# Performance work log

Hardware: AMD Instinct MI355X
Metric: run time of the kernel (lower is better)

Reference implementation:

```python
import jax, jax.numpy as jnp
import numpy as np

L = 2          # num_layers
B = 32         # batch
T = 64         # max_sequence_length (= source len here)
H = 1024       # hidden_size
E = 1024       # embedding_size (== H so layer weights stack uniformly)
V = 16000      # vocab (in == out)


def _cell(x, h, c, Wih, Whh, bih, bhh):
    # PyTorch LSTM gate order: i, f, g, o
    g = x @ Wih.T + h @ Whh.T + (bih + bhh)
    i, f, gg, o = jnp.split(g, 4, axis=-1)
    c_new = jax.nn.sigmoid(f) * c + jax.nn.sigmoid(i) * jnp.tanh(gg)
    h_new = jax.nn.sigmoid(o) * jnp.tanh(c_new)
    return h_new, c_new


def _stack_step(h, c, x, Wih, Whh, bih, bhh):
    # h, c: (L, B, H); x: (B, E). Fixed small loop over layers.
    hs, cs, inp = [], [], x
    for l in range(L):
        nh, nc = _cell(inp, h[l], c[l], Wih[l], Whh[l], bih[l], bhh[l])
        hs.append(nh); cs.append(nc); inp = nh
    return jnp.stack(hs), jnp.stack(cs), inp


def setup_inputs() -> dict:
    key = jax.random.key(0)
    ks = jax.random.split(key, 16)
    s = 1.0 / np.sqrt(H)
    U = lambda k, shp: jax.random.uniform(k, shp, jnp.float32, -s, s)
    inp = {
        "input_ids": jax.random.randint(ks[0], (B, T), 0, V),
        "output_ids": jax.random.randint(ks[1], (B, T), 0, V),
        "enc_emb": jax.random.normal(ks[2], (V, E), jnp.float32),
        "enc_Wih": U(ks[3], (L, 4 * H, H)),
        "enc_Whh": U(ks[4], (L, 4 * H, H)),
        "enc_bih": U(ks[5], (L, 4 * H)),
        "enc_bhh": U(ks[6], (L, 4 * H)),
        "dec_emb": jax.random.normal(ks[7], (V, E), jnp.float32),
        "dec_Wih": U(ks[8], (L, 4 * H, H)),
        "dec_Whh": U(ks[9], (L, 4 * H, H)),
        "dec_bih": U(ks[10], (L, 4 * H)),
        "dec_bhh": U(ks[11], (L, 4 * H)),
        "Wout": U(ks[12], (V, H)),
        "bout": U(ks[13], (V,)),
    }
    return inp


def reference(input_ids, output_ids, enc_emb, enc_Wih, enc_Whh, enc_bih, enc_bhh,
              dec_emb, dec_Wih, dec_Whh, dec_bih, dec_bhh, Wout, bout):
    dtype = enc_emb.dtype
    # ---- Encoder: run LSTM over source, keep final (h, c) ----
    enc_x = enc_emb[input_ids]                      # (B, T, E); dropout is identity (eval)
    h0 = jnp.zeros((L, B, H), dtype)
    c0 = jnp.zeros((L, B, H), dtype)

    def enc_step(carry, xt):
        h, c = carry
        h, c, _ = _stack_step(h, c, xt, enc_Wih, enc_Whh, enc_bih, enc_bhh)
        return (h, c), None

    (h, c), _ = jax.lax.scan(enc_step, (h0, c0), jnp.swapaxes(enc_x, 0, 1))

    # ---- Decoder: teacher-forced; step i consumes output_ids[:, i-1] ----
    dec_x = dec_emb[output_ids[:, : T - 1]]         # (B, T-1, E)

    def dec_step(carry, xt):
        h, c = carry
        h, c, top = _stack_step(h, c, xt, dec_Wih, dec_Whh, dec_bih, dec_bhh)
        logit = top @ Wout.T + bout                  # (B, V)
        return (h, c), logit

    (_, _), logits_seq = jax.lax.scan(dec_step, (h, c), jnp.swapaxes(dec_x, 0, 1))

    # ---- Assemble logits like the torch code ----
    logits = jnp.zeros((B, T, V), dtype)
    # torch: logits[:, 0, output_ids[:, 0]] = 1  (broadcasts over both batch dims)
    logits = logits.at[:, 0, output_ids[:, 0]].set(1.0)
    logits = logits.at[:, 1:, :].set(jnp.swapaxes(logits_seq, 0, 1))
    return logits
```

## Files before the change

kernel.cpp:

```cpp
#include <hip/hip_runtime.h>

namespace {

constexpr int kB = 32;
constexpr int kT = 64;
constexpr int kH = 1024;
constexpr int kE = 1024;
constexpr int kV = 16000;
constexpr int kG = 4096;

typedef __attribute__((ext_vector_type(8))) short short8v;
typedef __attribute__((ext_vector_type(4))) float f32x4;

__device__ __forceinline__ float sigmoid_f(float x) {
  return 1.0f / (1.0f + __expf(-x));
}
__device__ __forceinline__ unsigned short f2bf(float x) {
  unsigned int u = __builtin_bit_cast(unsigned int, x);
  u = (u + 0x7FFFu + ((u >> 16) & 1u)) >> 16;
  return (unsigned short)u;
}
__device__ __forceinline__ float bf2f(unsigned short h) {
  return __builtin_bit_cast(float, (unsigned int)h << 16);
}

__global__ void zero_t0_kernel(float* __restrict__ out) {
  int idx = blockIdx.x * blockDim.x + threadIdx.x;
  if (idx >= kB * kV) return;
  int b = idx / kV, v = idx % kV;
  __builtin_nontemporal_store(0.0f, &out[(size_t)b * kT * kV + v]);
}

__global__ void ones_t0_kernel(const int* __restrict__ output_ids,
                               float* __restrict__ out) {
  int b = threadIdx.x >> 5;
  int j = threadIdx.x & 31;
  int id = output_ids[j * kT];
  out[(size_t)b * kT * kV + id] = 1.0f;
}

struct ConvJobs {
  const float* src[8];
  unsigned short* dst[8];
  int mode[8];
};
__global__ __launch_bounds__(256)
void conv8(ConvJobs C) {
  const int mat = blockIdx.x >> 11;
  const int idx = (blockIdx.x & 2047) * 256 + threadIdx.x;
  const float* __restrict__ src = C.src[mat];
  unsigned short* __restrict__ dst = C.dst[mat];
  const int l = idx & 63;
  int row, k;
  if (C.mode[mat] == 0) {
    const int kstep = (idx >> 6) & 31;
    const int uq = (idx >> 11) & 1;
    const int ub = idx >> 12;
    const int n = l & 15;
    row = (n >> 2) * kH + ub * 8 + uq * 4 + (n & 3);
    k = kstep * 32 + ((l >> 4) << 3);
  } else {
    const int s = (idx >> 6) & 31;
    const int rg = idx >> 11;
    row = rg * 16 + (l & 15);
    k = s * 32 + ((l >> 4) << 3);
  }
  const float4* p = reinterpret_cast<const float4*>(src + (size_t)row * kH + k);
  float4 v0 = p[0], v1 = p[1];
  short8v o;
  o[0] = (short)f2bf(v0.x); o[1] = (short)f2bf(v0.y);
  o[2] = (short)f2bf(v0.z); o[3] = (short)f2bf(v0.w);
  o[4] = (short)f2bf(v1.x); o[5] = (short)f2bf(v1.y);
  o[6] = (short)f2bf(v1.z); o[7] = (short)f2bf(v1.w);
  *reinterpret_cast<short8v*>(dst + (size_t)idx * 8) = o;
}

__global__ __launch_bounds__(256)
void convert_frag(const float* __restrict__ src, unsigned short* __restrict__ dst,
                  int nchunks) {
  const int idx = blockIdx.x * 256 + threadIdx.x;
  if (idx >= nchunks) return;
  const int lane = idx & 63;
  const int s = (idx >> 6) & 31;
  const int rg = idx >> 11;
  const int row = rg * 16 + (lane & 15);
  const int k = s * 32 + ((lane >> 4) << 3);
  const float4* p = reinterpret_cast<const float4*>(src + (size_t)row * kH + k);
  float4 v0 = p[0], v1 = p[1];
  short8v o;
  o[0] = (short)f2bf(v0.x); o[1] = (short)f2bf(v0.y);
  o[2] = (short)f2bf(v0.z); o[3] = (short)f2bf(v0.w);
  o[4] = (short)f2bf(v1.x); o[5] = (short)f2bf(v1.y);
  o[6] = (short)f2bf(v1.z); o[7] = (short)f2bf(v1.w);
  *reinterpret_cast<short8v*>(dst + (size_t)idx * 8) = o;
}

__global__ void bias_cell(const float* __restrict__ bih,
                          const float* __restrict__ bhh, float* __restrict__ dst) {
  const int i = blockIdx.x * 256 + threadIdx.x;
  if (i >= kG) return;
  const int g = i >> 10, u = i & 1023;
  dst[(u >> 2) * 16 + g * 4 + (u & 3)] = bih[i] + bhh[i];
}

__global__ __launch_bounds__(256)
void gather_frag(const float* __restrict__ emb, const int* __restrict__ ids,
                 unsigned short* __restrict__ dst, int ntiles) {
  const int idx = blockIdx.x * 256 + threadIdx.x;
  const int lane = idx & 63;
  const int s = (idx >> 6) & 31;
  const int tile = idx >> 11;
  if (tile >= ntiles) return;
  const int m = tile * 16 + (lane & 15);
  const int t = m >> 5, b = m & 31;
  const int id = ids[b * kT + t];
  const int k = s * 32 + ((lane >> 4) << 3);
  const float4* p = reinterpret_cast<const float4*>(emb + (size_t)id * kE + k);
  float4 v0 = p[0], v1 = p[1];
  short8v o;
  o[0] = (short)f2bf(v0.x); o[1] = (short)f2bf(v0.y);
  o[2] = (short)f2bf(v0.z); o[3] = (short)f2bf(v0.w);
  o[4] = (short)f2bf(v1.x); o[5] = (short)f2bf(v1.y);
  o[6] = (short)f2bf(v1.z); o[7] = (short)f2bf(v1.w);
  *reinterpret_cast<short8v*>(dst + (size_t)idx * 8) = o;
}

__global__ __launch_bounds__(256)
void proj_mfma(const unsigned short* __restrict__ Af,
               const unsigned short* __restrict__ Bf,
               const float* __restrict__ b0, const float* __restrict__ b1,
               unsigned short* __restrict__ dst, int nmt) {
  const int w = threadIdx.x >> 6, lane = threadIdx.x & 63;
  const int mg = blockIdx.x, ng = blockIdx.y;
  f32x4 acc[4][2] = {};
  const unsigned short* Ab[4];
  const unsigned short* Bb[2];
#pragma unroll
  for (int i = 0; i < 4; ++i) {
    int tile = mg * 4 + i;
    if (tile > nmt - 1) tile = nmt - 1;
    Ab[i] = Af + (size_t)tile * 16384 + lane * 8;
  }
#pragma unroll
  for (int j = 0; j < 2; ++j) {
    const int nt = ng * 8 + w * 2 + j;
    Bb[j] = Bf + (size_t)nt * 16384 + lane * 8;
  }
#pragma unroll 2
  for (int s = 0; s < 32; ++s) {
    short8v a[4], b[2];
#pragma unroll
    for (int i = 0; i < 4; ++i) a[i] = *reinterpret_cast<const short8v*>(Ab[i] + s * 512);
#pragma unroll
    for (int j = 0; j < 2; ++j) b[j] = *reinterpret_cast<const short8v*>(Bb[j] + s * 512);
#pragma unroll
    for (int i = 0; i < 4; ++i)
#pragma unroll
      for (int j = 0; j < 2; ++j)
        acc[i][j] = __builtin_amdgcn_mfma_f32_16x16x32_bf16(a[i], b[j], acc[i][j], 0, 0, 0);
  }
#pragma unroll
  for (int i = 0; i < 4; ++i) {
    const int tile = mg * 4 + i;
    if (tile >= nmt) continue;
    const int mbase = tile * 16 + ((lane >> 4) << 2);
#pragma unroll
    for (int j = 0; j < 2; ++j) {
      const int n = (ng * 8 + w * 2 + j) * 16 + (lane & 15);
      const float bj = b0[n] + b1[n];
      const int g = n >> 10;
      const int u = n & 1023;
      const int q = u >> 2;
      const int uu = u & 3;
#pragma unroll
      for (int r = 0; r < 4; ++r) {
        const int m2 = mbase + r;
        const int t = m2 >> 5, mb = m2 & 31;
        dst[(size_t)t * kB * kG + (size_t)(q * 32 + mb) * 16 + g * 4 + uu] =
            f2bf(acc[i][j][r] + bj);
      }
    }
  }
}

__global__ __launch_bounds__(256)
void out_gemm_mfma(const unsigned short* __restrict__ Af,
                   const unsigned short* __restrict__ Bf,
                   const float* __restrict__ bias, float* __restrict__ out) {
  const int w = threadIdx.x >> 6, lane = threadIdx.x & 63;
  const int bid = blockIdx.x;
  const int swz = (bid & 7) * 252 + (bid >> 3);
  const int mg = swz & 31, ng = swz >> 5;
  __shared__ float LsF[32 * 260];
  f32x4 acc[4][4] = {};
  const unsigned short* Ab[4];
  const unsigned short* Bb[4];
#pragma unroll
  for (int i = 0; i < 4; ++i) {
    int tile = mg * 4 + i;
    if (tile > 125) tile = 125;
    Ab[i] = Af + (size_t)tile * 16384 + lane * 8;
  }
#pragma unroll
  for (int j = 0; j < 4; ++j) {
    int nt = ng * 16 + w * 4 + j;
    if (nt > 999) nt = 999;
    Bb[j] = Bf + (size_t)nt * 16384 + lane * 8;
  }
#pragma unroll 2
  for (int s = 0; s < 32; ++s) {
    short8v a[4], b[4];
#pragma unroll
    for (int i = 0; i < 4; ++i) a[i] = *reinterpret_cast<const short8v*>(Ab[i] + s * 512);
#pragma unroll
    for (int j = 0; j < 4; ++j) b[j] = *reinterpret_cast<const short8v*>(Bb[j] + s * 512);
#pragma unroll
    for (int i = 0; i < 4; ++i)
#pragma unroll
      for (int j = 0; j < 4; ++j)
        acc[i][j] = __builtin_amdgcn_mfma_f32_16x16x32_bf16(a[i], b[j], acc[i][j], 0, 0, 0);
  }
  const int nglob = ng * 256 + lane * 4;
  f32x4 b4 = {0.f, 0.f, 0.f, 0.f};
  if (nglob < kV) b4 = *reinterpret_cast<const f32x4*>(&bias[nglob]);
#pragma unroll
  for (int ph = 0; ph < 2; ++ph) {
    if (ph) __syncthreads();
#pragma unroll
    for (int i2 = 0; i2 < 2; ++i2) {
      const int i = ph * 2 + i2;
      const int r2b = i2 * 16 + ((lane >> 4) << 2);
#pragma unroll
      for (int j = 0; j < 4; ++j) {
        const int nloc = (w * 4 + j) * 16 + (lane & 15);
#pragma unroll
        for (int r = 0; r < 4; ++r) LsF[(r2b + r) * 260 + nloc] = acc[i][j][r];
      }
    }
    __syncthreads();
    if (nglob < kV) {
#pragma unroll
      for (int it = 0; it < 8; ++it) {
        const int r2l = w * 8 + it;
        const int m = mg * 64 + ph * 32 + r2l;
        if (m >= 2016) break;
        f32x4 v = *reinterpret_cast<const f32x4*>(&LsF[r2l * 260 + lane * 4]);
        v += b4;
        const int sd = m >> 5, bb = m & 31;
        f32x4* dst = reinterpret_cast<f32x4*>(
            &out[(size_t)bb * kT * kV + (size_t)(sd + 1) * kV + nglob]);
        __builtin_nontemporal_store(v, dst);
      }
    }
  }
}

struct RecurArgs {
  const unsigned short* wih1[2];
  const unsigned short* whh1[2];
  const unsigned short* whh0[2];
  const unsigned short* xproj[2];
  const float* bsum1[2];
  unsigned short* h0seq;
  unsigned short* h1seq;
  int* flags;
};

#define LOADW(dst, src)                                                      \
  {                                                                          \
    _Pragma("unroll") for (int s_ = 0; s_ < 4; ++s_) dst[s_] =               \
        *reinterpret_cast<const short8v*>((src) + wbase + (size_t)s_ * 512); \
  }

__global__ __launch_bounds__(512, 1)
void lstm_persist(RecurArgs A) {
  const int q = blockIdx.x;
  const int tid = threadIdx.x;
  const int wave = tid >> 6, lane = tid & 63;
  const int ksb = wave * 4;
  __shared__ alignas(16) float Ls[3][8][2][64][4];

  const size_t wbase = ((size_t)(q * 32 + ksb) * 64 + lane) * 8;
  short8v wI[4], wJ[4], wH[4];
  LOADW(wI, A.wih1[0]);
  LOADW(wJ, A.whh1[0]);
  LOADW(wH, A.whh0[0]);

  const int m = (tid < 128) ? (tid >> 2) : 0;
  const int ul = tid & 3;
  const int u = q * 4 + ul;
  float cold0 = 0.f, cold1 = 0.f;
  float bs[4];
  if (tid < 128) {
#pragma unroll
    for (int g = 0; g < 4; ++g) bs[g] = A.bsum1[0][q * 16 + g * 4 + ul];
  }
  const int mt = m >> 4, r = m & 3;
  const int lm = (m & 12) << 2;
  const int ksu = u >> 5;
  const int lane3 = (m & 15) | (((u >> 3) & 3) << 4);
  const int e = u & 7;
  const size_t fidx = (size_t)((mt * 32 + ksu) * 64 + lane3) * 8 + e;

  for (int p = 0; p < 128; ++p) {
    if (p == 64) LOADW(wH, A.whh0[1]);
    if (p == 65) {
      LOADW(wI, A.wih1[1]);
      LOADW(wJ, A.whh1[1]);
      if (tid < 128) {
#pragma unroll
        for (int g = 0; g < 4; ++g) bs[g] = A.bsum1[1][q * 16 + g * 4 + ul];
      }
    }
    float xp[4] = {};
    if (tid < 128 && p <= 126) {
      const int e0 = (p < kT) ? 0 : 1;
      const unsigned short* xprojc =
          A.xproj[e0] + (size_t)(e0 ? (p - kT) : p) * kB * kG;
#pragma unroll
      for (int g = 0; g < 4; ++g)
        xp[g] = bf2f(xprojc[(q * 32 + m) * 16 + g * 4 + ul]);
    }

    const unsigned short* A0 = A.h0seq + (size_t)p * 32768;
    const unsigned short* A1 = A.h1seq + (size_t)(p > 0 ? p - 1 : 0) * 32768;

    f32x4 aI0 = {0.f, 0.f, 0.f, 0.f}, aI1 = {0.f, 0.f, 0.f, 0.f};
    f32x4 aJ0 = {0.f, 0.f, 0.f, 0.f}, aJ1 = {0.f, 0.f, 0.f, 0.f};
    f32x4 aH0 = {0.f, 0.f, 0.f, 0.f}, aH1 = {0.f, 0.f, 0.f, 0.f};
#pragma unroll
    for (int s = 0; s < 4; ++s) {
      const int ks = ksb + s;
      const short8v a00 =
          *reinterpret_cast<const short8v*>(A0 + (size_t)(ks * 64 + lane) * 8);
      const short8v a01 =
          *reinterpret_cast<const short8v*>(A0 + (size_t)((32 + ks) * 64 + lane) * 8);
      const short8v a10 =
          *reinterpret_cast<const short8v*>(A1 + (size_t)(ks * 64 + lane) * 8);
      const short8v a11 =
          *reinterpret_cast<const short8v*>(A1 + (size_t)((32 + ks) * 64 + lane) * 8);
      aI0 = __builtin_amdgcn_mfma_f32_16x16x32_bf16(a00, wI[s], aI0, 0, 0, 0);
      aI1 = __builtin_amdgcn_mfma_f32_16x16x32_bf16(a01, wI[s], aI1, 0, 0, 0);
      aJ0 = __builtin_amdgcn_mfma_f32_16x16x32_bf16(a10, wJ[s], aJ0, 0, 0, 0);
      aJ1 = __builtin_amdgcn_mfma_f32_16x16x32_bf16(a11, wJ[s], aJ1, 0, 0, 0);
      aH0 = __builtin_amdgcn_mfma_f32_16x16x32_bf16(a00, wH[s], aH0, 0, 0, 0);
      aH1 = __builtin_amdgcn_mfma_f32_16x16x32_bf16(a01, wH[s], aH1, 0, 0, 0);
    }
    *reinterpret_cast<f32x4*>(&Ls[0][wave][0][lane][0]) = aI0;
    *reinterpret_cast<f32x4*>(&Ls[0][wave][1][lane][0]) = aI1;
    *reinterpret_cast<f32x4*>(&Ls[1][wave][0][lane][0]) = aJ0;
    *reinterpret_cast<f32x4*>(&Ls[1][wave][1][lane][0]) = aJ1;
    *reinterpret_cast<f32x4*>(&Ls[2][wave][0][lane][0]) = aH0;
    *reinterpret_cast<f32x4*>(&Ls[2][wave][1][lane][0]) = aH1;
    __syncthreads();

    if (tid < 128) {
      if (p <= 126) {
        float g0[4];
#pragma unroll
        for (int g = 0; g < 4; ++g) {
          const int ln = (g * 4 + ul) | lm;
          float v = 0.f;
#pragma unroll
          for (int ww = 0; ww < 8; ++ww) v += Ls[2][ww][mt][ln][r];
          g0[g] = v + xp[g];
        }
        const float cnew = sigmoid_f(g0[1]) * cold0 + sigmoid_f(g0[0]) * tanhf(g0[2]);
        const float hnew = sigmoid_f(g0[3]) * tanhf(cnew);
        cold0 = cnew;
        const unsigned int hb = f2bf(hnew);
        const unsigned int other = __shfl_xor((int)hb, 1);
        if ((ul & 1) == 0) {
          unsigned int word = (hb & 0xffffu) | (other << 16);
          unsigned int* dst = reinterpret_cast<unsigned int*>(
              A.h0seq + (size_t)(p + 1) * 32768 + fidx);
          __hip_atomic_store(dst, word, __ATOMIC_RELAXED,
                             __HIP_MEMORY_SCOPE_AGENT);
        }
      }
      if (p >= 1) {
        float g1[4];
#pragma unroll
        for (int g = 0; g < 4; ++g) {
          const int ln = (g * 4 + ul) | lm;
          float v = 0.f;
#pragma unroll
          for (int ww = 0; ww < 8; ++ww)
            v += Ls[0][ww][mt][ln][r] + Ls[1][ww][mt][ln][r];
          g1[g] = v + bs[g];
        }
        const float cnew = sigmoid_f(g1[1]) * cold1 + sigmoid_f(g1[0]) * tanhf(g1[2]);
        const float hnew = sigmoid_f(g1[3]) * tanhf(cnew);
        cold1 = cnew;
        const unsigned int hb = f2bf(hnew);
        const unsigned int other = __shfl_xor((int)hb, 1);
        if ((ul & 1) == 0) {
          unsigned int word = (hb & 0xffffu) | (other << 16);
          unsigned int* dst = reinterpret_cast<unsigned int*>(
              A.h1seq + (size_t)p * 32768 + fidx);
          __hip_atomic_store(dst, word, __ATOMIC_RELAXED,
                             __HIP_MEMORY_SCOPE_AGENT);
        }
      }
    }

    asm volatile("s_waitcnt vmcnt(0)" ::: "memory");
    __syncthreads();
    if (tid == 0)
      __hip_atomic_store(&A.flags[q], p + 1, __ATOMIC_RELAXED,
                         __HIP_MEMORY_SCOPE_AGENT);
    if (wave == 0) {
      const int fb = lane * 4;
      for (int guard = 0; guard < (1 << 17); ++guard) {
        int f0 = __hip_atomic_load(&A.flags[fb + 0], __ATOMIC_RELAXED,
                                   __HIP_MEMORY_SCOPE_AGENT);
        int f1 = __hip_atomic_load(&A.flags[fb + 1], __ATOMIC_RELAXED,
                                   __HIP_MEMORY_SCOPE_AGENT);
        int f2 = __hip_atomic_load(&A.flags[fb + 2], __ATOMIC_RELAXED,
                                   __HIP_MEMORY_SCOPE_AGENT);
        int f3 = __hip_atomic_load(&A.flags[fb + 3], __ATOMIC_RELAXED,
                                   __HIP_MEMORY_SCOPE_AGENT);
        const int mn = min(min(f0, f1), min(f2, f3));
        if (__all(mn > p)) break;
        __builtin_amdgcn_s_sleep(2);
      }
    }
    __syncthreads();
  }
}

}

extern "C" void kernel_launch(void* const* d_in, const int* in_sizes, int n_in,
                              void* d_out, int out_size, void* d_ws, size_t ws_size,
                              hipStream_t stream) {
  const int* input_ids = (const int*)d_in[0];
  const int* output_ids = (const int*)d_in[1];
  const float* enc_emb = (const float*)d_in[2];
  const float* enc_Wih = (const float*)d_in[3];
  const float* enc_Whh = (const float*)d_in[4];
  const float* enc_bih = (const float*)d_in[5];
  const float* enc_bhh = (const float*)d_in[6];
  const float* dec_emb = (const float*)d_in[7];
  const float* dec_Wih = (const float*)d_in[8];
  const float* dec_Whh = (const float*)d_in[9];
  const float* dec_bih = (const float*)d_in[10];
  const float* dec_bhh = (const float*)d_in[11];
  const float* Wout = (const float*)d_in[12];
  const float* bout = (const float*)d_in[13];
  float* out = (float*)d_out;
  char* ws = (char*)d_ws;

  const size_t WL = (size_t)kG * kH;

  size_t off = 0;
  unsigned short* wout_frag = (unsigned short*)(ws + 0);
  unsigned short* xproj_enc = (unsigned short*)(ws + off); off += (size_t)kT * kB * kG * 2;
  unsigned short* xin_enc = (unsigned short*)(ws + off);
  unsigned short* h0seq = xin_enc;
  off += (size_t)kT * kB * kH * 2;
  unsigned short* wih0_enc = (unsigned short*)(ws + off); off += WL * 2;
  unsigned short* wih0_dec = (unsigned short*)(ws + off); off += WL * 2;
  unsigned short* xproj_dec = (unsigned short*)(ws + off); off += (size_t)(kT - 1) * kB * kG * 2;
  unsigned short* xin_dec = (unsigned short*)(ws + off); off += (size_t)(kT - 1) * kB * kH * 2;
  unsigned short* h1seq = (unsigned short*)(ws + off); off += (size_t)128 * kB * kH * 2;
  unsigned short* wswz[6];
  for (int i = 0; i < 6; ++i) { wswz[i] = (unsigned short*)(ws + off); off += WL * 2; }
  float* bsum_enc = (float*)(ws + off); off += kG * 4;
  float* bsum_dec = (float*)(ws + off); off += kG * 4;
  int* flags = (int*)(ws + off); off += 1024;

  ConvJobs C;
  C.src[0] = enc_Whh;       C.dst[0] = wswz[0];    C.mode[0] = 0;
  C.src[1] = enc_Wih + WL;  C.dst[1] = wswz[1];    C.mode[1] = 0;
  C.src[2] = enc_Whh + WL;  C.dst[2] = wswz[2];    C.mode[2] = 0;
  C.src[3] = dec_Whh;       C.dst[3] = wswz[3];    C.mode[3] = 0;
  C.src[4] = dec_Wih + WL;  C.dst[4] = wswz[4];    C.mode[4] = 0;
  C.src[5] = dec_Whh + WL;  C.dst[5] = wswz[5];    C.mode[5] = 0;
  C.src[6] = enc_Wih;       C.dst[6] = wih0_enc;   C.mode[6] = 1;
  C.src[7] = dec_Wih;       C.dst[7] = wih0_dec;   C.mode[7] = 1;
  conv8<<<8 * 2048, 256, 0, stream>>>(C);
  bias_cell<<<16, 256, 0, stream>>>(enc_bih + kG, enc_bhh + kG, bsum_enc);
  bias_cell<<<16, 256, 0, stream>>>(dec_bih + kG, dec_bhh + kG, bsum_dec);

  gather_frag<<<128 * 8, 256, 0, stream>>>(enc_emb, input_ids, xin_enc, 128);
  gather_frag<<<126 * 8, 256, 0, stream>>>(dec_emb, output_ids, xin_dec, 126);

  proj_mfma<<<dim3(32, 32), 256, 0, stream>>>(xin_enc, wih0_enc, enc_bih, enc_bhh,
                                              xproj_enc, 128);
  proj_mfma<<<dim3(32, 32), 256, 0, stream>>>(xin_dec, wih0_dec, dec_bih, dec_bhh,
                                              xproj_dec, 126);

  (void)hipMemsetAsync(h0seq, 0, (size_t)kB * kH * 2, stream);
  (void)hipMemsetAsync(h1seq, 0, (size_t)kB * kH * 2, stream);
  (void)hipMemsetAsync(flags, 0, 1024, stream);

  RecurArgs RA;
  RA.wih1[0] = wswz[1]; RA.wih1[1] = wswz[4];
  RA.whh1[0] = wswz[2]; RA.whh1[1] = wswz[5];
  RA.whh0[0] = wswz[0]; RA.whh0[1] = wswz[3];
  RA.xproj[0] = xproj_enc; RA.xproj[1] = xproj_dec;
  RA.bsum1[0] = bsum_enc; RA.bsum1[1] = bsum_dec;
  RA.h0seq = h0seq;
  RA.h1seq = h1seq;
  RA.flags = flags;
  lstm_persist<<<256, 512, 0, stream>>>(RA);

  convert_frag<<<8000, 256, 0, stream>>>(Wout, wout_frag, kV * (kH / 8));

  zero_t0_kernel<<<(kB * kV + 255) / 256, 256, 0, stream>>>(out);
  ones_t0_kernel<<<1, kB * kB, 0, stream>>>(output_ids, out);

  out_gemm_mfma<<<2016, 256, 0, stream>>>(h1seq + (size_t)65 * kB * kH,
                                          wout_frag, bout, out);
}
```

Measured before the change: 1.178 ms.

## Use per-step atomic counter barrier and shrink output GEMM shared staging

```diff
diff --git a/kernel.cpp b/kernel.cpp
--- a/kernel.cpp
+++ b/kernel.cpp
@@ -183,7 +183,7 @@
   }
 }
 
-__global__ __launch_bounds__(256)
+__global__ __launch_bounds__(256, 5)
 void out_gemm_mfma(const unsigned short* __restrict__ Af,
                    const unsigned short* __restrict__ Bf,
                    const float* __restrict__ bias, float* __restrict__ out) {
@@ -191,7 +191,7 @@
   const int bid = blockIdx.x;
   const int swz = (bid & 7) * 252 + (bid >> 3);
   const int mg = swz & 31, ng = swz >> 5;
-  __shared__ float LsF[32 * 260];
+  __shared__ float LsF[16 * 260];
   f32x4 acc[4][4] = {};
   const unsigned short* Ab[4];
   const unsigned short* Bb[4];
@@ -224,32 +224,29 @@
   f32x4 b4 = {0.f, 0.f, 0.f, 0.f};
   if (nglob < kV) b4 = *reinterpret_cast<const f32x4*>(&bias[nglob]);
 #pragma unroll
-  for (int ph = 0; ph < 2; ++ph) {
-    if (ph) __syncthreads();
-#pragma unroll
-    for (int i2 = 0; i2 < 2; ++i2) {
-      const int i = ph * 2 + i2;
-      const int r2b = i2 * 16 + ((lane >> 4) << 2);
-#pragma unroll
-      for (int j = 0; j < 4; ++j) {
-        const int nloc = (w * 4 + j) * 16 + (lane & 15);
-#pragma unroll
-        for (int r = 0; r < 4; ++r) LsF[(r2b + r) * 260 + nloc] = acc[i][j][r];
-      }
+  for (int i = 0; i < 4; ++i) {
+    if (i) __syncthreads();
+    const int r2b = (lane >> 4) << 2;
+#pragma unroll
+    for (int j = 0; j < 4; ++j) {
+      const int nloc = (w * 4 + j) * 16 + (lane & 15);
+#pragma unroll
+      for (int r = 0; r < 4; ++r) LsF[(r2b + r) * 260 + nloc] = acc[i][j][r];
     }
     __syncthreads();
     if (nglob < kV) {
 #pragma unroll
-      for (int it = 0; it < 8; ++it) {
-        const int r2l = w * 8 + it;
-        const int m = mg * 64 + ph * 32 + r2l;
-        if (m >= 2016) break;
-        f32x4 v = *reinterpret_cast<const f32x4*>(&LsF[r2l * 260 + lane * 4]);
-        v += b4;
-        const int sd = m >> 5, bb = m & 31;
-        f32x4* dst = reinterpret_cast<f32x4*>(
-            &out[(size_t)bb * kT * kV + (size_t)(sd + 1) * kV + nglob]);
-        __builtin_nontemporal_store(v, dst);
+      for (int it = 0; it < 4; ++it) {
+        const int r2l = w * 4 + it;
+        const int m = mg * 64 + i * 16 + r2l;
+        if (m < 2016) {
+          f32x4 v = *reinterpret_cast<const f32x4*>(&LsF[r2l * 260 + lane * 4]);
+          v += b4;
+          const int sd = m >> 5, bb = m & 31;
+          f32x4* dst = reinterpret_cast<f32x4*>(
+              &out[(size_t)bb * kT * kV + (size_t)(sd + 1) * kV + nglob]);
+          __builtin_nontemporal_store(v, dst);
+        }
       }
     }
   }
@@ -263,7 +260,7 @@
   const float* bsum1[2];
   unsigned short* h0seq;
   unsigned short* h1seq;
-  int* flags;
+  int* ctr;
 };
 
 #define LOADW(dst, src)                                                      \
@@ -406,22 +403,13 @@
 
     asm volatile("s_waitcnt vmcnt(0)" ::: "memory");
     __syncthreads();
-    if (tid == 0)
-      __hip_atomic_store(&A.flags[q], p + 1, __ATOMIC_RELAXED,
-                         __HIP_MEMORY_SCOPE_AGENT);
-    if (wave == 0) {
-      const int fb = lane * 4;
-      for (int guard = 0; guard < (1 << 17); ++guard) {
-        int f0 = __hip_atomic_load(&A.flags[fb + 0], __ATOMIC_RELAXED,
-                                   __HIP_MEMORY_SCOPE_AGENT);
-        int f1 = __hip_atomic_load(&A.flags[fb + 1], __ATOMIC_RELAXED,
-                                   __HIP_MEMORY_SCOPE_AGENT);
-        int f2 = __hip_atomic_load(&A.flags[fb + 2], __ATOMIC_RELAXED,
-                                   __HIP_MEMORY_SCOPE_AGENT);
-        int f3 = __hip_atomic_load(&A.flags[fb + 3], __ATOMIC_RELAXED,
-                                   __HIP_MEMORY_SCOPE_AGENT);
-        const int mn = min(min(f0, f1), min(f2, f3));
-        if (__all(mn > p)) break;
+    if (tid == 0) {
+      __hip_atomic_fetch_add(&A.ctr[p * 16], 1, __ATOMIC_RELAXED,
+                             __HIP_MEMORY_SCOPE_AGENT);
+      for (int guard = 0; guard < (1 << 15); ++guard) {
+        const int v = __hip_atomic_load(&A.ctr[p * 16], __ATOMIC_RELAXED,
+                                        __HIP_MEMORY_SCOPE_AGENT);
+        if (v >= 256) break;
         __builtin_amdgcn_s_sleep(2);
       }
     }
@@ -468,7 +456,7 @@
   for (int i = 0; i < 6; ++i) { wswz[i] = (unsigned short*)(ws + off); off += WL * 2; }
   float* bsum_enc = (float*)(ws + off); off += kG * 4;
   float* bsum_dec = (float*)(ws + off); off += kG * 4;
-  int* flags = (int*)(ws + off); off += 1024;
+  int* ctr = (int*)(ws + off); off += 128 * 16 * 4;
 
   ConvJobs C;
   C.src[0] = enc_Whh;       C.dst[0] = wswz[0];    C.mode[0] = 0;
@@ -493,7 +481,7 @@
 
   (void)hipMemsetAsync(h0seq, 0, (size_t)kB * kH * 2, stream);
   (void)hipMemsetAsync(h1seq, 0, (size_t)kB * kH * 2, stream);
-  (void)hipMemsetAsync(flags, 0, 1024, stream);
+  (void)hipMemsetAsync(ctr, 0, 128 * 16 * 4, stream);
 
   RecurArgs RA;
   RA.wih1[0] = wswz[1]; RA.wih1[1] = wswz[4];
@@ -503,7 +491,7 @@
   RA.bsum1[0] = bsum_enc; RA.bsum1[1] = bsum_dec;
   RA.h0seq = h0seq;
   RA.h1seq = h1seq;
-  RA.flags = flags;
+  RA.ctr = ctr;
   lstm_persist<<<256, 512, 0, stream>>>(RA);
 
   convert_frag<<<8000, 256, 0, stream>>>(Wout, wout_frag, kV * (kH / 8));
```

After: 1.509 ms. +28.1%, slower.

## Split recurrence over batch halves and replace flag polling with hierarchical counter barrier

Applied to the files above, without the earlier changes.

```diff
diff --git a/kernel.cpp b/kernel.cpp
--- a/kernel.cpp
+++ b/kernel.cpp
@@ -263,40 +263,46 @@
   const float* bsum1[2];
   unsigned short* h0seq;
   unsigned short* h1seq;
-  int* flags;
+  int* xcnt;
+  int* gcnt;
 };
 
 #define LOADW(dst, src)                                                      \
   {                                                                          \
-    _Pragma("unroll") for (int s_ = 0; s_ < 4; ++s_) dst[s_] =               \
+    _Pragma("unroll") for (int s_ = 0; s_ < 8; ++s_) dst[s_] =               \
         *reinterpret_cast<const short8v*>((src) + wbase + (size_t)s_ * 512); \
   }
 
-__global__ __launch_bounds__(512, 1)
+__global__ __launch_bounds__(256)
 void lstm_persist(RecurArgs A) {
-  const int q = blockIdx.x;
+  const int bid = blockIdx.x;
+  const int q = (bid & 7) * 32 + ((bid >> 3) >> 1);
+  const int mt = (bid >> 3) & 1;
+  const int grp = bid >> 5;
   const int tid = threadIdx.x;
-  const int wave = tid >> 6, lane = tid & 63;
-  const int ksb = wave * 4;
-  __shared__ alignas(16) float Ls[3][8][2][64][4];
+  const int wave = tid >> 6;
+  const int lane = tid & 63;
+  const int ksb = wave * 8;
+  __shared__ alignas(16) float Ls[3][4][64][4];
 
   const size_t wbase = ((size_t)(q * 32 + ksb) * 64 + lane) * 8;
-  short8v wI[4], wJ[4], wH[4];
+  short8v wI[8], wJ[8], wH[8];
   LOADW(wI, A.wih1[0]);
   LOADW(wJ, A.whh1[0]);
   LOADW(wH, A.whh0[0]);
 
-  const int m = (tid < 128) ? (tid >> 2) : 0;
+  const int mloc = tid >> 2;
   const int ul = tid & 3;
+  const int m = mt * 16 + (mloc & 15);
   const int u = q * 4 + ul;
   float cold0 = 0.f, cold1 = 0.f;
-  float bs[4];
-  if (tid < 128) {
+  float bs[4] = {};
+  if (tid < 64) {
 #pragma unroll
     for (int g = 0; g < 4; ++g) bs[g] = A.bsum1[0][q * 16 + g * 4 + ul];
   }
-  const int mt = m >> 4, r = m & 3;
-  const int lm = (m & 12) << 2;
+  const int r = mloc & 3;
+  const int lm = (mloc & 12) << 2;
   const int ksu = u >> 5;
   const int lane3 = (m & 15) | (((u >> 3) & 3) << 4);
   const int e = u & 7;
@@ -307,13 +313,13 @@
     if (p == 65) {
       LOADW(wI, A.wih1[1]);
       LOADW(wJ, A.whh1[1]);
-      if (tid < 128) {
+      if (tid < 64) {
 #pragma unroll
         for (int g = 0; g < 4; ++g) bs[g] = A.bsum1[1][q * 16 + g * 4 + ul];
       }
     }
     float xp[4] = {};
-    if (tid < 128 && p <= 126) {
+    if (tid < 64 && p <= 126) {
       const int e0 = (p < kT) ? 0 : 1;
       const unsigned short* xprojc =
           A.xproj[e0] + (size_t)(e0 ? (p - kT) : p) * kB * kG;
@@ -325,45 +331,32 @@
     const unsigned short* A0 = A.h0seq + (size_t)p * 32768;
     const unsigned short* A1 = A.h1seq + (size_t)(p > 0 ? p - 1 : 0) * 32768;
 
-    f32x4 aI0 = {0.f, 0.f, 0.f, 0.f}, aI1 = {0.f, 0.f, 0.f, 0.f};
-    f32x4 aJ0 = {0.f, 0.f, 0.f, 0.f}, aJ1 = {0.f, 0.f, 0.f, 0.f};
-    f32x4 aH0 = {0.f, 0.f, 0.f, 0.f}, aH1 = {0.f, 0.f, 0.f, 0.f};
-#pragma unroll
-    for (int s = 0; s < 4; ++s) {
+    f32x4 aI = {0.f, 0.f, 0.f, 0.f};
+    f32x4 aJv = {0.f, 0.f, 0.f, 0.f};
+    f32x4 aH = {0.f, 0.f, 0.f, 0.f};
+#pragma unroll
+    for (int s = 0; s < 8; ++s) {
       const int ks = ksb + s;
-      const short8v a00 =
-          *reinterpret_cast<const short8v*>(A0 + (size_t)(ks * 64 + lane) * 8);
-      const short8v a01 =
-          *reinterpret_cast<const short8v*>(A0 + (size_t)((32 + ks) * 64 + lane) * 8);
-      const short8v a10 =
-          *reinterpret_cast<const short8v*>(A1 + (size_t)(ks * 64 + lane) * 8);
-      const short8v a11 =
-          *reinterpret_cast<const short8v*>(A1 + (size_t)((32 + ks) * 64 + lane) * 8);
-      aI0 = __builtin_amdgcn_mfma_f32_16x16x32_bf16(a00, wI[s], aI0, 0, 0, 0);
-      aI1 = __builtin_amdgcn_mfma_f32_16x16x32_bf16(a01, wI[s], aI1, 0, 0, 0);
-      aJ0 = __builtin_amdgcn_mfma_f32_16x16x32_bf16(a10, wJ[s], aJ0, 0, 0, 0);
-      aJ1 = __builtin_amdgcn_mfma_f32_16x16x32_bf16(a11, wJ[s], aJ1, 0, 0, 0);
-      aH0 = __builtin_amdgcn_mfma_f32_16x16x32_bf16(a00, wH[s], aH0, 0, 0, 0);
-      aH1 = __builtin_amdgcn_mfma_f32_16x16x32_bf16(a01, wH[s], aH1, 0, 0, 0);
-    }
-    *reinterpret_cast<f32x4*>(&Ls[0][wave][0][lane][0]) = aI0;
-    *reinterpret_cast<f32x4*>(&Ls[0][wave][1][lane][0]) = aI1;
-    *reinterpret_cast<f32x4*>(&Ls[1][wave][0][lane][0]) = aJ0;
-    *reinterpret_cast<f32x4*>(&Ls[1][wave][1][lane][0]) = aJ1;
-    *reinterpret_cast<f32x4*>(&Ls[2][wave][0][lane][0]) = aH0;
-    *reinterpret_cast<f32x4*>(&Ls[2][wave][1][lane][0]) = aH1;
+      const size_t aidx = (size_t)((mt * 32 + ks) * 64 + lane) * 8;
+      const short8v a0 = *reinterpret_cast<const short8v*>(A0 + aidx);
+      const short8v a1 = *reinterpret_cast<const short8v*>(A1 + aidx);
+      aI = __builtin_amdgcn_mfma_f32_16x16x32_bf16(a0, wI[s], aI, 0, 0, 0);
+      aJv = __builtin_amdgcn_mfma_f32_16x16x32_bf16(a1, wJ[s], aJv, 0, 0, 0);
+      aH = __builtin_amdgcn_mfma_f32_16x16x32_bf16(a0, wH[s], aH, 0, 0, 0);
+    }
+    *reinterpret_cast<f32x4*>(&Ls[0][wave][lane][0]) = aI;
+    *reinterpret_cast<f32x4*>(&Ls[1][wave][lane][0]) = aJv;
+    *reinterpret_cast<f32x4*>(&Ls[2][wave][lane][0]) = aH;
     __syncthreads();
 
-    if (tid < 128) {
+    if (tid < 64) {
       if (p <= 126) {
         float g0[4];
 #pragma unroll
         for (int g = 0; g < 4; ++g) {
           const int ln = (g * 4 + ul) | lm;
-          float v = 0.f;
-#pragma unroll
-          for (int ww = 0; ww < 8; ++ww) v += Ls[2][ww][mt][ln][r];
-          g0[g] = v + xp[g];
+          g0[g] = Ls[2][0][ln][r] + Ls[2][1][ln][r] + Ls[2][2][ln][r] +
+                  Ls[2][3][ln][r] + xp[g];
         }
         const float cnew = sigmoid_f(g0[1]) * cold0 + sigmoid_f(g0[0]) * tanhf(g0[2]);
         const float hnew = sigmoid_f(g0[3]) * tanhf(cnew);
@@ -383,11 +376,9 @@
 #pragma unroll
         for (int g = 0; g < 4; ++g) {
           const int ln = (g * 4 + ul) | lm;
-          float v = 0.f;
-#pragma unroll
-          for (int ww = 0; ww < 8; ++ww)
-            v += Ls[0][ww][mt][ln][r] + Ls[1][ww][mt][ln][r];
-          g1[g] = v + bs[g];
+          g1[g] = Ls[0][0][ln][r] + Ls[0][1][ln][r] + Ls[0][2][ln][r] +
+                  Ls[0][3][ln][r] + Ls[1][0][ln][r] + Ls[1][1][ln][r] +
+                  Ls[1][2][ln][r] + Ls[1][3][ln][r] + bs[g];
         }
         const float cnew = sigmoid_f(g1[1]) * cold1 + sigmoid_f(g1[0]) * tanhf(g1[2]);
         const float hnew = sigmoid_f(g1[3]) * tanhf(cnew);
@@ -406,23 +397,18 @@
 
     asm volatile("s_waitcnt vmcnt(0)" ::: "memory");
     __syncthreads();
-    if (tid == 0)
-      __hip_atomic_store(&A.flags[q], p + 1, __ATOMIC_RELAXED,
-                         __HIP_MEMORY_SCOPE_AGENT);
-    if (wave == 0) {
-      const int fb = lane * 4;
-      for (int guard = 0; guard < (1 << 17); ++guard) {
-        int f0 = __hip_atomic_load(&A.flags[fb + 0], __ATOMIC_RELAXED,
-                                   __HIP_MEMORY_SCOPE_AGENT);
-        int f1 = __hip_atomic_load(&A.flags[fb + 1], __ATOMIC_RELAXED,
-                                   __HIP_MEMORY_SCOPE_AGENT);
-        int f2 = __hip_atomic_load(&A.flags[fb + 2], __ATOMIC_RELAXED,
-                                   __HIP_MEMORY_SCOPE_AGENT);
-        int f3 = __hip_atomic_load(&A.flags[fb + 3], __ATOMIC_RELAXED,
-                                   __HIP_MEMORY_SCOPE_AGENT);
-        const int mn = min(min(f0, f1), min(f2, f3));
-        if (__all(mn > p)) break;
-        __builtin_amdgcn_s_sleep(2);
+    if (tid == 0) {
+      const int a =
+          __hip_atomic_fetch_add(&A.xcnt[(p * 16 + grp) * 32], 1,
+                                 __ATOMIC_RELAXED, __HIP_MEMORY_SCOPE_AGENT);
+      if (a == 31)
+        __hip_atomic_fetch_add(&A.gcnt[p * 32], 1, __ATOMIC_RELAXED,
+                               __HIP_MEMORY_SCOPE_AGENT);
+      for (int guard = 0; guard < (1 << 14); ++guard) {
+        const int v = __hip_atomic_load(&A.gcnt[p * 32], __ATOMIC_RELAXED,
+                                        __HIP_MEMORY_SCOPE_AGENT);
+        if (v >= 16) break;
+        __builtin_amdgcn_s_sleep(1);
       }
     }
     __syncthreads();
@@ -468,7 +454,8 @@
   for (int i = 0; i < 6; ++i) { wswz[i] = (unsigned short*)(ws + off); off += WL * 2; }
   float* bsum_enc = (float*)(ws + off); off += kG * 4;
   float* bsum_dec = (float*)(ws + off); off += kG * 4;
-  int* flags = (int*)(ws + off); off += 1024;
+  int* xcnt = (int*)(ws + off); off += 128 * 16 * 32 * 4;
+  int* gcnt = (int*)(ws + off); off += 128 * 32 * 4;
 
   ConvJobs C;
   C.src[0] = enc_Whh;       C.dst[0] = wswz[0];    C.mode[0] = 0;
@@ -493,7 +480,7 @@
 
   (void)hipMemsetAsync(h0seq, 0, (size_t)kB * kH * 2, stream);
   (void)hipMemsetAsync(h1seq, 0, (size_t)kB * kH * 2, stream);
-  (void)hipMemsetAsync(flags, 0, 1024, stream);
+  (void)hipMemsetAsync(xcnt, 0, (128 * 16 * 32 + 128 * 32) * 4, stream);
 
   RecurArgs RA;
   RA.wih1[0] = wswz[1]; RA.wih1[1] = wswz[4];
@@ -503,8 +490,9 @@
   RA.bsum1[0] = bsum_enc; RA.bsum1[1] = bsum_dec;
   RA.h0seq = h0seq;
   RA.h1seq = h1seq;
-  RA.flags = flags;
-  lstm_persist<<<256, 512, 0, stream>>>(RA);
+  RA.xcnt = xcnt;
+  RA.gcnt = gcnt;
+  lstm_persist<<<512, 256, 0, stream>>>(RA);
 
   convert_frag<<<8000, 256, 0, stream>>>(Wout, wout_frag, kV * (kH / 8));
 
```

After: 1.198 ms. About the same (+1.7%).
